# Optimization experiments

Measured on AMD Instinct MI355X. Metric: run time of the kernel, lower is better.

## Reference

```python
import jax, jax.numpy as jnp
import numpy as np

LN_EPS = 1e-5


def setup_inputs() -> dict:
    key = jax.random.key(0)
    k1, k2, k3, k4, k5 = jax.random.split(key, 5)
    V, D_REAL, D_HID, D_MODEL = 32000, 768, 512, 4096
    B, S = 4, 2048
    return {
        "real": jax.random.normal(k1, (V, D_REAL), dtype=jnp.float32),
        "llama_embed": jax.random.normal(k2, (V, D_MODEL), dtype=jnp.float32),
        "w1": jax.random.normal(k3, (D_HID, D_REAL), dtype=jnp.float32),  # trans_1.weight
        "w2": jax.random.normal(k4, (D_MODEL, D_HID), dtype=jnp.float32),  # trans_2.weight
        "ln_w": jnp.ones((D_HID,), dtype=jnp.float32),
        "ln_b": jnp.zeros((D_HID,), dtype=jnp.float32),
        "input_ids": jax.random.randint(k5, (B, S), 0, V, dtype=jnp.int64),
    }


def _layernorm(x, w, b):
    mu = jnp.mean(x, axis=-1, keepdims=True)
    var = jnp.mean(jnp.square(x - mu), axis=-1, keepdims=True)
    return (x - mu) * jax.lax.rsqrt(var + LN_EPS) * w + b


def reference(real, llama_embed, w1, w2, ln_w, ln_b, input_ids):
    # trans_2(ELU(LayerNorm(trans_1(real)))) over the FULL table, as in the original
    h = jnp.einsum("vd,hd->vh", real, w1)            # [V, 512]
    h = jax.nn.elu(_layernorm(h, ln_w, ln_b))        # [V, 512]
    transfered = jnp.einsum("vh,mh->vm", h, w2)      # [V, 4096]
    # gather rows per token and add frozen llama embeddings
    return transfered[input_ids] + llama_embed[input_ids]  # [B, S, 4096]
```

## Files before the change

kernel.cpp:

```cpp
#include <hip/hip_runtime.h>
#include <hip/hip_bf16.h>
#include <math.h>

#define TOKENS 8192
#define D_REAL 768
#define D_HID  512
#define D_MODEL 4096

typedef __attribute__((ext_vector_type(8))) short bf16x8;
typedef __attribute__((ext_vector_type(4))) float f32x4;

__device__ inline unsigned short f2bf(float f) {
    union { float f; unsigned u; } v; v.f = f;
    unsigned r = v.u + 0x7FFFu + ((v.u >> 16) & 1u);
    return (unsigned short)(r >> 16);
}
__device__ inline float bf2f(unsigned short h) {
    union { unsigned u; float f; } v; v.u = ((unsigned)h) << 16;
    return v.f;
}

__device__ inline void gload_lds16(const void* g, void* lds_wave_base) {
    __builtin_amdgcn_global_load_lds(
        (const __attribute__((address_space(1))) unsigned*)g,
        (__attribute__((address_space(3))) unsigned*)lds_wave_base,
        16, 0, 0);
}

__global__ __launch_bounds__(256)
void gemm1_mfma(const unsigned short* __restrict__ A,
                const unsigned short* __restrict__ B,
                unsigned short* __restrict__ C)
{
    constexpr int K = D_REAL, N = D_HID;
    __shared__ __align__(16) unsigned short As[64 * 32];
    __shared__ __align__(16) unsigned short Bs[128 * 32];

    const int tid = threadIdx.x;
    const int rowBase = blockIdx.x * 64;
    const int colBase = blockIdx.y * 128;

    const int srow = tid >> 2;
    const int scol = (tid & 3) * 8;
    const unsigned short* gA = A + (size_t)(rowBase + srow) * K + scol;
    const unsigned short* gB = B + (size_t)(colBase + srow) * K + scol;
    unsigned short* lA = As + (tid >> 6) * 512;
    unsigned short* lB = Bs + (tid >> 6) * 512;

    const int lane = tid & 63;
    const int wv   = tid >> 6;
    const int wm   = (wv >> 1) * 32;
    const int wn   = (wv & 1) * 64;
    const int frow = lane & 15;
    const int fk   = (lane >> 4) * 8;

    f32x4 acc[2][4];
    #pragma unroll
    for (int i = 0; i < 2; i++)
        #pragma unroll
        for (int j = 0; j < 4; j++) acc[i][j] = (f32x4)0.f;

    for (int k0 = 0; k0 < K; k0 += 32) {
        gload_lds16(gA,                lA);
        gload_lds16(gB,                lB);
        gload_lds16(gB + (size_t)64*K, lB + 2048);
        gA += 32; gB += 32;
        __syncthreads();

        bf16x8 af[2], bg[4];
        #pragma unroll
        for (int i = 0; i < 2; i++)
            af[i] = *reinterpret_cast<const bf16x8*>(&As[(wm + i*16 + frow) * 32 + fk]);
        #pragma unroll
        for (int j = 0; j < 4; j++)
            bg[j] = *reinterpret_cast<const bf16x8*>(&Bs[(wn + j*16 + frow) * 32 + fk]);

        #pragma unroll
        for (int i = 0; i < 2; i++)
            #pragma unroll
            for (int j = 0; j < 4; j++)
                acc[i][j] = __builtin_amdgcn_mfma_f32_16x16x32_bf16(af[i], bg[j], acc[i][j], 0, 0, 0);
        __syncthreads();
    }

    const int orow0 = wm + (lane >> 4) * 4;
    const int ocol0 = wn + frow;
    #pragma unroll
    for (int i = 0; i < 2; i++)
        #pragma unroll
        for (int r = 0; r < 4; r++) {
            unsigned short* dst = C + (size_t)(rowBase + orow0 + i*16 + r) * N + colBase + ocol0;
            #pragma unroll
            for (int j = 0; j < 4; j++)
                dst[j * 16] = f2bf(acc[i][j][r]);
        }
}

__global__ __launch_bounds__(256)
void gemm2_mfma(const unsigned short* __restrict__ A,
                const unsigned short* __restrict__ B,
                const int* __restrict__ ids,
                const float* __restrict__ embed,
                float* __restrict__ C)
{
    constexpr int K = D_HID, N = D_MODEL;
    __shared__ __align__(16) unsigned char smem[32 * 132 * 4];
    unsigned short* As = (unsigned short*)smem;
    unsigned short* Bs = (unsigned short*)(smem + 8192);
    float* Ct = (float*)smem;
    __shared__ int sIds[128];

    const int tid = threadIdx.x;
    const int rowBase = blockIdx.x * 128;
    const int colBase = blockIdx.y * 128;

    if (tid < 128) sIds[tid] = ids[rowBase + tid];

    const int srow = tid >> 2;
    const int scol = (tid & 3) * 8;
    const unsigned short* gA = A + (size_t)(rowBase + srow) * K + scol;
    const unsigned short* gB = B + (size_t)(colBase + srow) * K + scol;
    unsigned short* lA = As + (tid >> 6) * 512;
    unsigned short* lB = Bs + (tid >> 6) * 512;

    const int lane = tid & 63;
    const int wv   = tid >> 6;
    const int wm   = (wv >> 1) * 64;
    const int wn   = (wv & 1) * 64;
    const int frow = lane & 15;
    const int fk   = (lane >> 4) * 8;

    f32x4 acc[4][4];
    #pragma unroll
    for (int i = 0; i < 4; i++)
        #pragma unroll
        for (int j = 0; j < 4; j++) acc[i][j] = (f32x4)0.f;

    for (int k0 = 0; k0 < K; k0 += 32) {
        gload_lds16(gA,                lA);
        gload_lds16(gA + (size_t)64*K, lA + 2048);
        gload_lds16(gB,                lB);
        gload_lds16(gB + (size_t)64*K, lB + 2048);
        gA += 32; gB += 32;
        __syncthreads();

        bf16x8 af[4], bg[4];
        #pragma unroll
        for (int i = 0; i < 4; i++)
            af[i] = *reinterpret_cast<const bf16x8*>(&As[(wm + i*16 + frow) * 32 + fk]);
        #pragma unroll
        for (int j = 0; j < 4; j++)
            bg[j] = *reinterpret_cast<const bf16x8*>(&Bs[(wn + j*16 + frow) * 32 + fk]);

        #pragma unroll
        for (int i = 0; i < 4; i++)
            #pragma unroll
            for (int j = 0; j < 4; j++)
                acc[i][j] = __builtin_amdgcn_mfma_f32_16x16x32_bf16(af[i], bg[j], acc[i][j], 0, 0, 0);
        __syncthreads();
    }

    const int rl_w = (wv >> 1) * 16 + (lane >> 4) * 4;
    const int rl_r = tid >> 3;
    const int cs   = (tid & 7) * 16;
    #pragma unroll
    for (int c = 0; c < 4; c++) {
        if (c) __syncthreads();
        #pragma unroll
        for (int r = 0; r < 4; r++)
            #pragma unroll
            for (int j = 0; j < 4; j++)
                Ct[(rl_w + r) * 132 + wn + frow + j * 16] = acc[c][j][r];
        __syncthreads();
        const int gr = (rl_r & 15) + c * 16 + (rl_r >> 4) * 64;
        const float* e = embed + (size_t)sIds[gr] * N + colBase + cs;
        float* dst = C + (size_t)(rowBase + gr) * N + colBase + cs;
        #pragma unroll
        for (int q = 0; q < 4; q++) {
            float4 v = *reinterpret_cast<const float4*>(&Ct[rl_r * 132 + cs + q * 4]);
            const float4 ev = *reinterpret_cast<const float4*>(e + q * 4);
            v.x += ev.x; v.y += ev.y; v.z += ev.z; v.w += ev.w;
            *reinterpret_cast<float4*>(dst + q * 4) = v;
        }
    }
}

__global__ __launch_bounds__(256)
void convert_bf16(const float* __restrict__ src, unsigned short* __restrict__ dst, int n4)
{
    const int i = blockIdx.x * 256 + threadIdx.x;
    if (i >= n4) return;
    const float4 v = reinterpret_cast<const float4*>(src)[i];
    ushort4 o;
    o.x = f2bf(v.x); o.y = f2bf(v.y); o.z = f2bf(v.z); o.w = f2bf(v.w);
    reinterpret_cast<ushort4*>(dst)[i] = o;
}

__global__ __launch_bounds__(192)
void gather_bf16(const float* __restrict__ real, const int* __restrict__ ids,
                 unsigned short* __restrict__ Ag)
{
    const int row = blockIdx.x;
    const int t = threadIdx.x;
    const float4 v = *reinterpret_cast<const float4*>(real + (size_t)ids[row] * D_REAL + t * 4);
    ushort4 o;
    o.x = f2bf(v.x); o.y = f2bf(v.y); o.z = f2bf(v.z); o.w = f2bf(v.w);
    *reinterpret_cast<ushort4*>(Ag + (size_t)row * D_REAL + t * 4) = o;
}

__global__ __launch_bounds__(256)
void ln_elu_bf16(unsigned short* __restrict__ H,
                 const float* __restrict__ ln_w, const float* __restrict__ ln_b)
{
    const int row = blockIdx.x * 4 + (threadIdx.x >> 6);
    const int t = threadIdx.x & 63;
    unsigned short* x = H + (size_t)row * D_HID + t * 8;

    bf16x8 v = *reinterpret_cast<const bf16x8*>(x);
    float f[8], s = 0.f, ss = 0.f;
    #pragma unroll
    for (int j = 0; j < 8; j++) {
        f[j] = bf2f((unsigned short)v[j]);
        s += f[j]; ss += f[j] * f[j];
    }
    #pragma unroll
    for (int off = 32; off > 0; off >>= 1) {
        s  += __shfl_down(s, off);
        ss += __shfl_down(ss, off);
    }
    s = __shfl(s, 0); ss = __shfl(ss, 0);
    const float mu = s * (1.f / D_HID);
    const float var = ss * (1.f / D_HID) - mu * mu;
    const float rstd = rsqrtf(var + 1e-5f);

    const float4 w0 = *reinterpret_cast<const float4*>(ln_w + t * 8);
    const float4 w1 = *reinterpret_cast<const float4*>(ln_w + t * 8 + 4);
    const float4 b0 = *reinterpret_cast<const float4*>(ln_b + t * 8);
    const float4 b1 = *reinterpret_cast<const float4*>(ln_b + t * 8 + 4);
    const float wa[8] = { w0.x, w0.y, w0.z, w0.w, w1.x, w1.y, w1.z, w1.w };
    const float ba[8] = { b0.x, b0.y, b0.z, b0.w, b1.x, b1.y, b1.z, b1.w };

    bf16x8 o;
    #pragma unroll
    for (int j = 0; j < 8; j++) {
        float y = (f[j] - mu) * rstd * wa[j] + ba[j];
        y = y > 0.f ? y : expm1f(y);
        o[j] = (short)f2bf(y);
    }
    *reinterpret_cast<bf16x8*>(x) = o;
}

extern "C" void kernel_launch(void* const* d_in, const int* in_sizes, int n_in,
                              void* d_out, int out_size, void* d_ws, size_t ws_size,
                              hipStream_t stream)
{
    const float* real  = (const float*)d_in[0];
    const float* embed = (const float*)d_in[1];
    const float* w1    = (const float*)d_in[2];
    const float* w2    = (const float*)d_in[3];
    const float* ln_w  = (const float*)d_in[4];
    const float* ln_b  = (const float*)d_in[5];
    const int*   ids   = (const int*)d_in[6];
    float* out = (float*)d_out;

    unsigned short* Hb  = (unsigned short*)d_ws;
    unsigned short* w1b = Hb  + (size_t)TOKENS * D_HID;
    unsigned short* w2b = w1b + (size_t)D_HID * D_REAL;
    unsigned short* Ag  = (unsigned short*)d_out;

    convert_bf16<<<(D_HID * D_REAL / 4 + 255) / 256, 256, 0, stream>>>(w1, w1b, D_HID * D_REAL / 4);
    convert_bf16<<<(D_MODEL * D_HID / 4 + 255) / 256, 256, 0, stream>>>(w2, w2b, D_MODEL * D_HID / 4);
    gather_bf16<<<TOKENS, 192, 0, stream>>>(real, ids, Ag);

    dim3 g1(TOKENS / 64, D_HID / 128);
    gemm1_mfma<<<g1, 256, 0, stream>>>(Ag, w1b, Hb);

    ln_elu_bf16<<<TOKENS / 4, 256, 0, stream>>>(Hb, ln_w, ln_b);

    dim3 g2(TOKENS / 128, D_MODEL / 128);
    gemm2_mfma<<<g2, 256, 0, stream>>>(Hb, w2b, ids, embed, out);
}
```

Measured before the change: 146.6 us.

## Remap gemm2 blocks per XCD, write epilogue directly, fuse weight conversions

```diff
diff --git a/kernel.cpp b/kernel.cpp
--- a/kernel.cpp
+++ b/kernel.cpp
@@ -104,16 +104,17 @@
                 float* __restrict__ C)
 {
     constexpr int K = D_HID, N = D_MODEL;
-    __shared__ __align__(16) unsigned char smem[32 * 132 * 4];
-    unsigned short* As = (unsigned short*)smem;
-    unsigned short* Bs = (unsigned short*)(smem + 8192);
-    float* Ct = (float*)smem;
+    __shared__ __align__(16) unsigned short As[128 * 32];
+    __shared__ __align__(16) unsigned short Bs[128 * 32];
     __shared__ int sIds[128];
 
+    const int f   = blockIdx.x;
+    const int xcd = f & 7;
+    const int idx = f >> 3;
+    const int rowBase = (xcd * 8 + (idx & 7)) * 128;
+    const int colBase = (idx >> 3) * 128;
+
     const int tid = threadIdx.x;
-    const int rowBase = blockIdx.x * 128;
-    const int colBase = blockIdx.y * 128;
-
     if (tid < 128) sIds[tid] = ids[rowBase + tid];
 
     const int srow = tid >> 2;
@@ -160,36 +161,34 @@
         __syncthreads();
     }
 
-    const int rl_w = (wv >> 1) * 16 + (lane >> 4) * 4;
-    const int rl_r = tid >> 3;
-    const int cs   = (tid & 7) * 16;
-    #pragma unroll
-    for (int c = 0; c < 4; c++) {
-        if (c) __syncthreads();
-        #pragma unroll
-        for (int r = 0; r < 4; r++)
-            #pragma unroll
-            for (int j = 0; j < 4; j++)
-                Ct[(rl_w + r) * 132 + wn + frow + j * 16] = acc[c][j][r];
-        __syncthreads();
-        const int gr = (rl_r & 15) + c * 16 + (rl_r >> 4) * 64;
-        const float* e = embed + (size_t)sIds[gr] * N + colBase + cs;
-        float* dst = C + (size_t)(rowBase + gr) * N + colBase + cs;
-        #pragma unroll
-        for (int q = 0; q < 4; q++) {
-            float4 v = *reinterpret_cast<const float4*>(&Ct[rl_r * 132 + cs + q * 4]);
-            const float4 ev = *reinterpret_cast<const float4*>(e + q * 4);
-            v.x += ev.x; v.y += ev.y; v.z += ev.z; v.w += ev.w;
-            *reinterpret_cast<float4*>(dst + q * 4) = v;
+    const int orow0 = wm + (lane >> 4) * 4;
+    const int ocol0 = wn + frow;
+    #pragma unroll
+    for (int i = 0; i < 4; i++) {
+        #pragma unroll
+        for (int r = 0; r < 4; r++) {
+            const int lrow = orow0 + i * 16 + r;
+            const size_t grow = (size_t)(rowBase + lrow);
+            const float* e = embed + (size_t)sIds[lrow] * N + colBase + ocol0;
+            #pragma unroll
+            for (int j = 0; j < 4; j++)
+                C[grow * N + colBase + ocol0 + j * 16] = acc[i][j][r] + e[j * 16];
         }
     }
 }
 
 __global__ __launch_bounds__(256)
-void convert_bf16(const float* __restrict__ src, unsigned short* __restrict__ dst, int n4)
-{
-    const int i = blockIdx.x * 256 + threadIdx.x;
-    if (i >= n4) return;
+void convert2_bf16(const float* __restrict__ s1, unsigned short* __restrict__ d1, int n1,
+                   const float* __restrict__ s2, unsigned short* __restrict__ d2, int n2)
+{
+    int i = blockIdx.x * 256 + threadIdx.x;
+    const float* src; unsigned short* dst;
+    if (i < n1) { src = s1; dst = d1; }
+    else {
+        i -= n1;
+        if (i >= n2) return;
+        src = s2; dst = d2;
+    }
     const float4 v = reinterpret_cast<const float4*>(src)[i];
     ushort4 o;
     o.x = f2bf(v.x); o.y = f2bf(v.y); o.z = f2bf(v.z); o.w = f2bf(v.w);
@@ -268,8 +267,8 @@
     unsigned short* w2b = w1b + (size_t)D_HID * D_REAL;
     unsigned short* Ag  = (unsigned short*)d_out;
 
-    convert_bf16<<<(D_HID * D_REAL / 4 + 255) / 256, 256, 0, stream>>>(w1, w1b, D_HID * D_REAL / 4);
-    convert_bf16<<<(D_MODEL * D_HID / 4 + 255) / 256, 256, 0, stream>>>(w2, w2b, D_MODEL * D_HID / 4);
+    const int n1 = D_HID * D_REAL / 4, n2 = D_MODEL * D_HID / 4;
+    convert2_bf16<<<(n1 + n2 + 255) / 256, 256, 0, stream>>>(w1, w1b, n1, w2, w2b, n2);
     gather_bf16<<<TOKENS, 192, 0, stream>>>(real, ids, Ag);
 
     dim3 g1(TOKENS / 64, D_HID / 128);
@@ -277,6 +276,5 @@
 
     ln_elu_bf16<<<TOKENS / 4, 256, 0, stream>>>(Hb, ln_w, ln_b);
 
-    dim3 g2(TOKENS / 128, D_MODEL / 128);
-    gemm2_mfma<<<g2, 256, 0, stream>>>(Hb, w2b, ids, embed, out);
-}
+    gemm2_mfma<<<2048, 256, 0, stream>>>(Hb, w2b, ids, embed, out);
+}
```

Measured after the change: 129.0 us. 12.0% less time.
